# Performance work log

Measured on AMD Instinct MI355X. Metric: run time of the kernel, lower is better.

## Reference

```python
import jax, jax.numpy as jnp
import numpy as np

N_NODES = 100000
N_EDGES = 1600000
D = 128
L = 3


def setup_inputs() -> dict:
    key = jax.random.key(0)
    ks = jax.random.split(key, 5)
    x = jax.random.normal(ks[0], (N_NODES, D), dtype=jnp.float32)
    # Xavier-ish scale for stability through 3 layers
    scale = 1.0 / np.sqrt(D)
    W_self = jax.random.normal(ks[1], (L, D, D), dtype=jnp.float32) * scale
    W_neigh = jax.random.normal(ks[2], (L, D, D), dtype=jnp.float32) * scale
    bias = jnp.zeros((L, D), dtype=jnp.float32)
    src = jax.random.randint(ks[3], (N_EDGES,), 0, N_NODES)
    dst = jax.random.randint(ks[4], (N_EDGES,), 0, N_NODES)
    return {"x": x, "W_self": W_self, "W_neigh": W_neigh, "bias": bias,
            "src": src, "dst": dst}


def reference(x, W_self, W_neigh, bias, src, dst):
    """HomoSAGEEncoder forward (inference mode, dropout = identity).

    Each layer: DGL SAGEConv('mean'):
        h_neigh[v] = mean_{u in in-neighbors(v)} h[u]   (0 if no neighbors)
        h = h @ W_self + h_neigh @ W_neigh + bias
    followed by ReLU.
    """
    N = x.shape[0]
    n_layers = W_self.shape[0]
    # in-degree per destination node (shared across layers)
    deg = jax.ops.segment_sum(jnp.ones_like(dst, dtype=x.dtype), dst,
                              num_segments=N)
    inv_deg = (1.0 / jnp.maximum(deg, 1.0))[:, None]  # [N,1]

    h = x
    for l in range(n_layers):
        msg = h[src]  # [E,D] gather
        h_neigh = jax.ops.segment_sum(msg, dst, num_segments=N) * inv_deg
        h = h @ W_self[l] + h_neigh @ W_neigh[l] + bias[l]
        h = jax.nn.relu(h)
        # dropout is identity at inference; skipped
    return h
```

## Files before the change

### kernel.cpp

```cpp
#include <hip/hip_runtime.h>

typedef __attribute__((ext_vector_type(8))) short short8;
typedef __attribute__((ext_vector_type(4))) float f32x4;

static constexpr int NN = 100000;
static constexpr int NE = 1600000;
static constexpr int DD = 128;
static constexpr int NBUCK = 196;
static constexpr int CAP = 9216;

static constexpr int OFF_GCUR  = 0;
static constexpr int OFF_BBASE = 256;
static constexpr int OFF_OFFS  = 512;
static constexpr int OFF_INV   = 100516;
static constexpr int OFF_WT    = 200520;
static constexpr int OFF_SS    = 249680;
static constexpr int OFF_HB    = 1849680;
static constexpr int OFF_HNB   = 8249680;

__device__ inline ushort f2b(float f) {
  uint u = __builtin_bit_cast(uint, f);
  uint r = (u + 0x7fffu + ((u >> 16) & 1u)) >> 16;
  return (ushort)r;
}
__device__ inline float b2f(ushort b) {
  uint u = ((uint)b) << 16;
  return __builtin_bit_cast(float, u);
}

__global__ void k_zero(int* p) {
  int i = blockIdx.x * blockDim.x + threadIdx.x;
  if (i < 256) p[i] = 0;
}

__global__ void k_x2b(const float* __restrict__ x, ushort* __restrict__ hb) {
  int i = blockIdx.x * blockDim.x + threadIdx.x;
  if (i < NN * (DD / 2)) {
    float2 v = *(const float2*)(x + (size_t)i * 2);
    uint p = (uint)f2b(v.x) | ((uint)f2b(v.y) << 16);
    *(uint*)(hb + (size_t)i * 2) = p;
  }
}

__global__ void k_wt(const float* __restrict__ Ws, const float* __restrict__ Wn,
                     ushort* __restrict__ WtP) {
  int i = blockIdx.x * blockDim.x + threadIdx.x;
  if (i < 3 * 8 * 128 * 32) {
    int j = i & 7;
    int kg = (i >> 3) & 3;
    int col = (i >> 5) & 127;
    int kt = (i >> 12) & 7;
    int l = i >> 15;
    int k = kt * 32 + kg * 8 + j;
    float v = (k < 128) ? Ws[((size_t)l * 128 + k) * 128 + col]
                        : Wn[((size_t)l * 128 + (k - 128)) * 128 + col];
    WtP[i] = f2b(v);
  }
}

__global__ __launch_bounds__(256) void k_bucket(const int* __restrict__ src,
                                                const int* __restrict__ dst,
                                                int* __restrict__ gcur,
                                                int2* __restrict__ ebuf) {
  __shared__ int cnt[NBUCK], base[NBUCK];
  int t = threadIdx.x;
  int b0 = blockIdx.x * 4096;
  if (t < NBUCK) cnt[t] = 0;
  __syncthreads();
  int dv[16], pv[16];
#pragma unroll
  for (int j = 0; j < 16; ++j) {
    int idx = b0 + j * 256 + t;
    if (idx < NE) {
      int d = dst[idx];
      dv[j] = d;
      pv[j] = atomicAdd(&cnt[d >> 9], 1);
    } else dv[j] = -1;
  }
  __syncthreads();
  if (t < NBUCK) base[t] = atomicAdd(&gcur[t], cnt[t]);
  __syncthreads();
#pragma unroll
  for (int j = 0; j < 16; ++j) {
    if (dv[j] >= 0) {
      int idx = b0 + j * 256 + t;
      int b = dv[j] >> 9;
      int2 pr; pr.x = src[idx]; pr.y = dv[j];
      ebuf[(size_t)b * CAP + base[b] + pv[j]] = pr;
    }
  }
}

__global__ void k_bscan(const int* __restrict__ gcur, int* __restrict__ bbase) {
  __shared__ int sc[256];
  int t = threadIdx.x;
  int v = (t < NBUCK) ? gcur[t] : 0;
  sc[t] = v;
  __syncthreads();
  for (int off = 1; off < 256; off <<= 1) {
    int u = (t >= off) ? sc[t - off] : 0;
    __syncthreads();
    sc[t] += u;
    __syncthreads();
  }
  if (t < NBUCK) bbase[t] = sc[t] - v;
  if (t == 255) bbase[NBUCK] = sc[255];
}

__global__ __launch_bounds__(256) void k_sort(const int2* __restrict__ ebuf,
                                              const int* __restrict__ bbase,
                                              int* __restrict__ offs,
                                              float* __restrict__ inv,
                                              int* __restrict__ ss) {
  __shared__ int cnt[512];
  __shared__ int sbase[512];
  __shared__ int scan[256];
  __shared__ int sarr[CAP];
  int b = blockIdx.x, t = threadIdx.x;
  int base0 = bbase[b];
  int n = bbase[b + 1] - base0;
  cnt[t] = 0; cnt[t + 256] = 0;
  __syncthreads();
  const int2* eb = ebuf + (size_t)b * CAP;
  for (int i = t; i < n; i += 256) atomicAdd(&cnt[eb[i].y & 511], 1);
  __syncthreads();
  int c0 = cnt[2 * t], c1 = cnt[2 * t + 1];
  int s = c0 + c1;
  scan[t] = s;
  __syncthreads();
  for (int off = 1; off < 256; off <<= 1) {
    int u = (t >= off) ? scan[t - off] : 0;
    __syncthreads();
    scan[t] += u;
    __syncthreads();
  }
  int eb2 = scan[t] - s;
  sbase[2 * t] = eb2;
  sbase[2 * t + 1] = eb2 + c0;
  int g0 = b * 512 + 2 * t, g1 = g0 + 1;
  if (g0 < NN) {
    offs[g0] = base0 + eb2;
    inv[g0] = 1.0f / (float)(c0 > 1 ? c0 : 1);
  }
  if (g1 < NN) {
    offs[g1] = base0 + eb2 + c0;
    inv[g1] = 1.0f / (float)(c1 > 1 ? c1 : 1);
  }
  if (b == NBUCK - 1 && t == 0) offs[NN] = NE;
  cnt[2 * t] = 0; cnt[2 * t + 1] = 0;
  __syncthreads();
  for (int i = t; i < n; i += 256) {
    int2 e = eb[i];
    int ln = e.y & 511;
    int p = sbase[ln] + atomicAdd(&cnt[ln], 1);
    sarr[p] = e.x;
  }
  __syncthreads();
  for (int i = t; i < n; i += 256) ss[base0 + i] = sarr[i];
}

__global__ __launch_bounds__(256) void k_agg3(const ushort* __restrict__ h,
                                              const int* __restrict__ offs,
                                              const int* __restrict__ ss,
                                              const float* __restrict__ inv_deg,
                                              ushort* __restrict__ hN) {
  int gid = blockIdx.x * blockDim.x + threadIdx.x;
  int wid = gid >> 6;
  int lane = threadIdx.x & 63;
  int q = lane >> 4, l16 = lane & 15;
  int v = wid * 4 + q;
  int beg = offs[v], end = offs[v + 1];
  float a0 = 0, a1 = 0, a2 = 0, a3 = 0, a4 = 0, a5 = 0, a6 = 0, a7 = 0;
  const ushort* hp = h + (size_t)l16 * 8;
#define ACC8(u) { a0 += b2f((ushort)u.x); a1 += b2f((ushort)(u.x >> 16)); \
                  a2 += b2f((ushort)u.y); a3 += b2f((ushort)(u.y >> 16)); \
                  a4 += b2f((ushort)u.z); a5 += b2f((ushort)(u.z >> 16)); \
                  a6 += b2f((ushort)u.w); a7 += b2f((ushort)(u.w >> 16)); }
  int e = beg;
  for (; e + 7 < end; e += 8) {
    uint4 u0 = *(const uint4*)(hp + (size_t)ss[e + 0] * DD);
    uint4 u1 = *(const uint4*)(hp + (size_t)ss[e + 1] * DD);
    uint4 u2 = *(const uint4*)(hp + (size_t)ss[e + 2] * DD);
    uint4 u3 = *(const uint4*)(hp + (size_t)ss[e + 3] * DD);
    uint4 u4 = *(const uint4*)(hp + (size_t)ss[e + 4] * DD);
    uint4 u5 = *(const uint4*)(hp + (size_t)ss[e + 5] * DD);
    uint4 u6 = *(const uint4*)(hp + (size_t)ss[e + 6] * DD);
    uint4 u7 = *(const uint4*)(hp + (size_t)ss[e + 7] * DD);
    ACC8(u0) ACC8(u1) ACC8(u2) ACC8(u3) ACC8(u4) ACC8(u5) ACC8(u6) ACC8(u7)
  }
  for (; e < end; ++e) {
    uint4 u0 = *(const uint4*)(hp + (size_t)ss[e] * DD);
    ACC8(u0)
  }
#undef ACC8
  float w = inv_deg[v];
  a0 *= w; a1 *= w; a2 *= w; a3 *= w; a4 *= w; a5 *= w; a6 *= w; a7 *= w;
  uint4 p;
  p.x = (uint)f2b(a0) | ((uint)f2b(a1) << 16);
  p.y = (uint)f2b(a2) | ((uint)f2b(a3) << 16);
  p.z = (uint)f2b(a4) | ((uint)f2b(a5) << 16);
  p.w = (uint)f2b(a6) | ((uint)f2b(a7) << 16);
  *(uint4*)(hN + (size_t)v * DD + l16 * 8) = p;
}

__global__ __launch_bounds__(256) void k_gemm2(
    const ushort* __restrict__ hA, const ushort* __restrict__ hNb,
    const ushort* __restrict__ WtP, const float* __restrict__ bias,
    ushort* __restrict__ hOutB, float* __restrict__ outF, int writeF) {
  int w = threadIdx.x >> 6;
  int lane = threadIdx.x & 63;
  int r = lane & 15, kg = lane >> 4;
  int colbase = w * 32;

  short8 bfrag[8][2];
#pragma unroll
  for (int kt = 0; kt < 8; ++kt)
#pragma unroll
    for (int nt = 0; nt < 2; ++nt) {
      int col = colbase + nt * 16 + r;
      bfrag[kt][nt] = *(const short8*)(WtP + ((size_t)(kt * 128 + col) * 4 + kg) * 8);
    }

  float bv[2];
  bv[0] = bias[colbase + r];
  bv[1] = bias[colbase + 16 + r];

  int rowblk = blockIdx.x * 128;
#pragma unroll 1
  for (int half = 0; half < 2; ++half) {
    f32x4 acc[2][2][2];
#pragma unroll
    for (int it = 0; it < 2; ++it) {
      int row0 = rowblk + half * 64 + it * 32;
      int ra0 = row0 + r;      if (ra0 > NN - 1) ra0 = NN - 1;
      int ra1 = row0 + 16 + r; if (ra1 > NN - 1) ra1 = NN - 1;
#pragma unroll
      for (int mt = 0; mt < 2; ++mt)
#pragma unroll
        for (int nt = 0; nt < 2; ++nt) acc[it][mt][nt] = (f32x4)0.f;
#pragma unroll
      for (int kt = 0; kt < 8; ++kt) {
        const ushort* hs = (kt < 4) ? hA : hNb;
        int kk = (kt & 3) * 32 + kg * 8;
        short8 a0 = *(const short8*)(hs + (size_t)ra0 * DD + kk);
        short8 a1 = *(const short8*)(hs + (size_t)ra1 * DD + kk);
        acc[it][0][0] = __builtin_amdgcn_mfma_f32_16x16x32_bf16(a0, bfrag[kt][0], acc[it][0][0], 0, 0, 0);
        acc[it][0][1] = __builtin_amdgcn_mfma_f32_16x16x32_bf16(a0, bfrag[kt][1], acc[it][0][1], 0, 0, 0);
        acc[it][1][0] = __builtin_amdgcn_mfma_f32_16x16x32_bf16(a1, bfrag[kt][0], acc[it][1][0], 0, 0, 0);
        acc[it][1][1] = __builtin_amdgcn_mfma_f32_16x16x32_bf16(a1, bfrag[kt][1], acc[it][1][1], 0, 0, 0);
      }
    }
    __syncthreads();
#pragma unroll
    for (int it = 0; it < 2; ++it) {
      int row0 = rowblk + half * 64 + it * 32;
#pragma unroll
      for (int mt = 0; mt < 2; ++mt) {
#pragma unroll
        for (int j = 0; j < 4; ++j) {
          int row = row0 + mt * 16 + kg * 4 + j;
          if (row < NN) {
#pragma unroll
            for (int nt = 0; nt < 2; ++nt) {
              float val = fmaxf(acc[it][mt][nt][j] + bv[nt], 0.f);
              int col = colbase + nt * 16 + r;
              hOutB[(size_t)row * DD + col] = f2b(val);
              if (writeF) outF[(size_t)row * DD + col] = val;
            }
          }
        }
      }
    }
    __syncthreads();
  }
}

extern "C" void kernel_launch(void* const* d_in, const int* in_sizes, int n_in,
                              void* d_out, int out_size, void* d_ws, size_t ws_size,
                              hipStream_t stream) {
  const float* x    = (const float*)d_in[0];
  const float* Ws   = (const float*)d_in[1];
  const float* Wn   = (const float*)d_in[2];
  const float* bias = (const float*)d_in[3];
  const int*   src  = (const int*)d_in[4];
  const int*   dst  = (const int*)d_in[5];
  float* out = (float*)d_out;

  int* ws      = (int*)d_ws;
  int* gcur    = ws + OFF_GCUR;
  int* bbase   = ws + OFF_BBASE;
  int* offs    = ws + OFF_OFFS;
  float* inv   = (float*)(ws + OFF_INV);
  ushort* WtP  = (ushort*)(ws + OFF_WT);
  int* ssorted = ws + OFF_SS;
  ushort* hB   = (ushort*)(ws + OFF_HB);
  ushort* hNb  = (ushort*)(ws + OFF_HNB);
  int2* ebuf   = (int2*)(ws + OFF_HNB);

  k_zero<<<1, 256, 0, stream>>>(gcur);
  k_x2b<<<(NN * (DD / 2) + 255) / 256, 256, 0, stream>>>(x, hB);
  k_wt<<<(3 * 8 * 128 * 32 + 255) / 256, 256, 0, stream>>>(Ws, Wn, WtP);
  k_bucket<<<(NE + 4095) / 4096, 256, 0, stream>>>(src, dst, gcur, ebuf);
  k_bscan<<<1, 256, 0, stream>>>(gcur, bbase);
  k_sort<<<NBUCK, 256, 0, stream>>>(ebuf, bbase, offs, inv, ssorted);

  for (int l = 0; l < 3; ++l) {
    k_agg3<<<NN / 4 / 4, 256, 0, stream>>>(hB, offs, ssorted, inv, hNb);
    k_gemm2<<<(NN + 127) / 128, 256, 0, stream>>>(
        hB, hNb, WtP + (size_t)l * 8 * 128 * 32, bias + l * DD, hB, out, l == 2 ? 1 : 0);
  }
}
```

Before: 531.3 us.

## Fuse neighbor aggregation into GEMM via LDS and merge setup kernels

```diff
diff --git a/kernel.cpp b/kernel.cpp
--- a/kernel.cpp
+++ b/kernel.cpp
@@ -9,14 +9,13 @@
 static constexpr int NBUCK = 196;
 static constexpr int CAP = 9216;
 
-static constexpr int OFF_GCUR  = 0;
-static constexpr int OFF_BBASE = 256;
-static constexpr int OFF_OFFS  = 512;
-static constexpr int OFF_INV   = 100516;
-static constexpr int OFF_WT    = 200520;
-static constexpr int OFF_SS    = 249680;
-static constexpr int OFF_HB    = 1849680;
-static constexpr int OFF_HNB   = 8249680;
+static constexpr int OFF_GCUR = 0;
+static constexpr int OFF_OFFS = 512;
+static constexpr int OFF_INV  = 100516;
+static constexpr int OFF_WT   = 200520;
+static constexpr int OFF_SS   = 249680;
+static constexpr int OFF_HB   = 1849680;
+static constexpr int OFF_HC   = 8249680;
 
 __device__ inline ushort f2b(float f) {
   uint u = __builtin_bit_cast(uint, f);
@@ -28,24 +27,22 @@
   return __builtin_bit_cast(float, u);
 }
 
-__global__ void k_zero(int* p) {
-  int i = blockIdx.x * blockDim.x + threadIdx.x;
-  if (i < 256) p[i] = 0;
-}
-
-__global__ void k_x2b(const float* __restrict__ x, ushort* __restrict__ hb) {
-  int i = blockIdx.x * blockDim.x + threadIdx.x;
-  if (i < NN * (DD / 2)) {
-    float2 v = *(const float2*)(x + (size_t)i * 2);
-    uint p = (uint)f2b(v.x) | ((uint)f2b(v.y) << 16);
-    *(uint*)(hb + (size_t)i * 2) = p;
-  }
-}
-
-__global__ void k_wt(const float* __restrict__ Ws, const float* __restrict__ Wn,
-                     ushort* __restrict__ WtP) {
-  int i = blockIdx.x * blockDim.x + threadIdx.x;
-  if (i < 3 * 8 * 128 * 32) {
+__global__ __launch_bounds__(256) void k_pre(const float* __restrict__ x,
+                                             const float* __restrict__ Ws,
+                                             const float* __restrict__ Wn,
+                                             ushort* __restrict__ hb,
+                                             ushort* __restrict__ WtP,
+                                             int* __restrict__ gcur) {
+  int b = blockIdx.x, t = threadIdx.x;
+  if (b < 12500) {
+    int i = b * 256 + t;
+    float4 v = *(const float4*)(x + (size_t)i * 4);
+    uint2 p;
+    p.x = (uint)f2b(v.x) | ((uint)f2b(v.y) << 16);
+    p.y = (uint)f2b(v.z) | ((uint)f2b(v.w) << 16);
+    *(uint2*)(hb + (size_t)i * 4) = p;
+  } else if (b < 12884) {
+    int i = (b - 12500) * 256 + t;
     int j = i & 7;
     int kg = (i >> 3) & 3;
     int col = (i >> 5) & 127;
@@ -55,6 +52,8 @@
     float v = (k < 128) ? Ws[((size_t)l * 128 + k) * 128 + col]
                         : Wn[((size_t)l * 128 + (k - 128)) * 128 + col];
     WtP[i] = f2b(v);
+  } else {
+    gcur[t] = 0;
   }
 }
 
@@ -91,24 +90,8 @@
   }
 }
 
-__global__ void k_bscan(const int* __restrict__ gcur, int* __restrict__ bbase) {
-  __shared__ int sc[256];
-  int t = threadIdx.x;
-  int v = (t < NBUCK) ? gcur[t] : 0;
-  sc[t] = v;
-  __syncthreads();
-  for (int off = 1; off < 256; off <<= 1) {
-    int u = (t >= off) ? sc[t - off] : 0;
-    __syncthreads();
-    sc[t] += u;
-    __syncthreads();
-  }
-  if (t < NBUCK) bbase[t] = sc[t] - v;
-  if (t == 255) bbase[NBUCK] = sc[255];
-}
-
 __global__ __launch_bounds__(256) void k_sort(const int2* __restrict__ ebuf,
-                                              const int* __restrict__ bbase,
+                                              const int* __restrict__ gcur,
                                               int* __restrict__ offs,
                                               float* __restrict__ inv,
                                               int* __restrict__ ss) {
@@ -117,8 +100,18 @@
   __shared__ int scan[256];
   __shared__ int sarr[CAP];
   int b = blockIdx.x, t = threadIdx.x;
-  int base0 = bbase[b];
-  int n = bbase[b + 1] - base0;
+  int gv = (t < NBUCK) ? gcur[t] : 0;
+  scan[t] = gv;
+  __syncthreads();
+  for (int off = 1; off < 256; off <<= 1) {
+    int u = (t >= off) ? scan[t - off] : 0;
+    __syncthreads();
+    scan[t] += u;
+    __syncthreads();
+  }
+  int nB = gcur[b];
+  int base0 = scan[b] - nB;
+  int n = nB;
   cnt[t] = 0; cnt[t + 256] = 0;
   __syncthreads();
   const int2* eb = ebuf + (size_t)b * CAP;
@@ -159,120 +152,121 @@
   for (int i = t; i < n; i += 256) ss[base0 + i] = sarr[i];
 }
 
-__global__ __launch_bounds__(256) void k_agg3(const ushort* __restrict__ h,
-                                              const int* __restrict__ offs,
-                                              const int* __restrict__ ss,
-                                              const float* __restrict__ inv_deg,
-                                              ushort* __restrict__ hN) {
-  int gid = blockIdx.x * blockDim.x + threadIdx.x;
-  int wid = gid >> 6;
-  int lane = threadIdx.x & 63;
-  int q = lane >> 4, l16 = lane & 15;
-  int v = wid * 4 + q;
-  int beg = offs[v], end = offs[v + 1];
-  float a0 = 0, a1 = 0, a2 = 0, a3 = 0, a4 = 0, a5 = 0, a6 = 0, a7 = 0;
-  const ushort* hp = h + (size_t)l16 * 8;
+__global__ __launch_bounds__(256) void k_fused(
+    const ushort* __restrict__ hIn, const int* __restrict__ offs,
+    const int* __restrict__ ss, const float* __restrict__ inv_deg,
+    const ushort* __restrict__ WtP, const float* __restrict__ bias,
+    ushort* __restrict__ hOut, float* __restrict__ outF, int writeF) {
+  __shared__ ushort hN[128 * 128];
+  int t = threadIdx.x;
+  int w = t >> 6, lane = t & 63;
+  int r = lane & 15, kg = lane >> 4;
+  int row0 = blockIdx.x * 128;
+
+  int colbase = w * 32;
+  short8 bfrag[8][2];
+#pragma unroll
+  for (int kt = 0; kt < 8; ++kt)
+#pragma unroll
+    for (int nt = 0; nt < 2; ++nt) {
+      int col = colbase + nt * 16 + r;
+      bfrag[kt][nt] = *(const short8*)(WtP + ((size_t)(kt * 128 + col) * 4 + kg) * 8);
+    }
+  float bv[2];
+  bv[0] = bias[colbase + r];
+  bv[1] = bias[colbase + 16 + r];
+
+  const ushort* hp = hIn + (size_t)r * 8;
+#pragma unroll 1
+  for (int g = 0; g < 8; ++g) {
+    int lr = w * 32 + g * 4 + kg;
+    int v = row0 + lr;
+    float a0 = 0, a1 = 0, a2 = 0, a3 = 0, a4 = 0, a5 = 0, a6 = 0, a7 = 0;
+    if (v < NN) {
+      int beg = offs[v], end = offs[v + 1];
 #define ACC8(u) { a0 += b2f((ushort)u.x); a1 += b2f((ushort)(u.x >> 16)); \
                   a2 += b2f((ushort)u.y); a3 += b2f((ushort)(u.y >> 16)); \
                   a4 += b2f((ushort)u.z); a5 += b2f((ushort)(u.z >> 16)); \
                   a6 += b2f((ushort)u.w); a7 += b2f((ushort)(u.w >> 16)); }
-  int e = beg;
-  for (; e + 7 < end; e += 8) {
-    uint4 u0 = *(const uint4*)(hp + (size_t)ss[e + 0] * DD);
-    uint4 u1 = *(const uint4*)(hp + (size_t)ss[e + 1] * DD);
-    uint4 u2 = *(const uint4*)(hp + (size_t)ss[e + 2] * DD);
-    uint4 u3 = *(const uint4*)(hp + (size_t)ss[e + 3] * DD);
-    uint4 u4 = *(const uint4*)(hp + (size_t)ss[e + 4] * DD);
-    uint4 u5 = *(const uint4*)(hp + (size_t)ss[e + 5] * DD);
-    uint4 u6 = *(const uint4*)(hp + (size_t)ss[e + 6] * DD);
-    uint4 u7 = *(const uint4*)(hp + (size_t)ss[e + 7] * DD);
-    ACC8(u0) ACC8(u1) ACC8(u2) ACC8(u3) ACC8(u4) ACC8(u5) ACC8(u6) ACC8(u7)
-  }
-  for (; e < end; ++e) {
-    uint4 u0 = *(const uint4*)(hp + (size_t)ss[e] * DD);
-    ACC8(u0)
-  }
+      int e = beg;
+      for (; e + 7 < end; e += 8) {
+        uint4 u0 = *(const uint4*)(hp + (size_t)ss[e + 0] * DD);
+        uint4 u1 = *(const uint4*)(hp + (size_t)ss[e + 1] * DD);
+        uint4 u2 = *(const uint4*)(hp + (size_t)ss[e + 2] * DD);
+        uint4 u3 = *(const uint4*)(hp + (size_t)ss[e + 3] * DD);
+        uint4 u4 = *(const uint4*)(hp + (size_t)ss[e + 4] * DD);
+        uint4 u5 = *(const uint4*)(hp + (size_t)ss[e + 5] * DD);
+        uint4 u6 = *(const uint4*)(hp + (size_t)ss[e + 6] * DD);
+        uint4 u7 = *(const uint4*)(hp + (size_t)ss[e + 7] * DD);
+        ACC8(u0) ACC8(u1) ACC8(u2) ACC8(u3) ACC8(u4) ACC8(u5) ACC8(u6) ACC8(u7)
+      }
+      for (; e < end; ++e) {
+        uint4 u0 = *(const uint4*)(hp + (size_t)ss[e] * DD);
+        ACC8(u0)
+      }
 #undef ACC8
-  float w = inv_deg[v];
-  a0 *= w; a1 *= w; a2 *= w; a3 *= w; a4 *= w; a5 *= w; a6 *= w; a7 *= w;
-  uint4 p;
-  p.x = (uint)f2b(a0) | ((uint)f2b(a1) << 16);
-  p.y = (uint)f2b(a2) | ((uint)f2b(a3) << 16);
-  p.z = (uint)f2b(a4) | ((uint)f2b(a5) << 16);
-  p.w = (uint)f2b(a6) | ((uint)f2b(a7) << 16);
-  *(uint4*)(hN + (size_t)v * DD + l16 * 8) = p;
-}
-
-__global__ __launch_bounds__(256) void k_gemm2(
-    const ushort* __restrict__ hA, const ushort* __restrict__ hNb,
-    const ushort* __restrict__ WtP, const float* __restrict__ bias,
-    ushort* __restrict__ hOutB, float* __restrict__ outF, int writeF) {
-  int w = threadIdx.x >> 6;
-  int lane = threadIdx.x & 63;
-  int r = lane & 15, kg = lane >> 4;
-  int colbase = w * 32;
-
-  short8 bfrag[8][2];
-#pragma unroll
-  for (int kt = 0; kt < 8; ++kt)
-#pragma unroll
-    for (int nt = 0; nt < 2; ++nt) {
-      int col = colbase + nt * 16 + r;
-      bfrag[kt][nt] = *(const short8*)(WtP + ((size_t)(kt * 128 + col) * 4 + kg) * 8);
+      float sc = inv_deg[v];
+      a0 *= sc; a1 *= sc; a2 *= sc; a3 *= sc;
+      a4 *= sc; a5 *= sc; a6 *= sc; a7 *= sc;
     }
-
-  float bv[2];
-  bv[0] = bias[colbase + r];
-  bv[1] = bias[colbase + 16 + r];
-
-  int rowblk = blockIdx.x * 128;
-#pragma unroll 1
-  for (int half = 0; half < 2; ++half) {
-    f32x4 acc[2][2][2];
-#pragma unroll
-    for (int it = 0; it < 2; ++it) {
-      int row0 = rowblk + half * 64 + it * 32;
-      int ra0 = row0 + r;      if (ra0 > NN - 1) ra0 = NN - 1;
-      int ra1 = row0 + 16 + r; if (ra1 > NN - 1) ra1 = NN - 1;
-#pragma unroll
-      for (int mt = 0; mt < 2; ++mt)
-#pragma unroll
-        for (int nt = 0; nt < 2; ++nt) acc[it][mt][nt] = (f32x4)0.f;
-#pragma unroll
-      for (int kt = 0; kt < 8; ++kt) {
-        const ushort* hs = (kt < 4) ? hA : hNb;
-        int kk = (kt & 3) * 32 + kg * 8;
-        short8 a0 = *(const short8*)(hs + (size_t)ra0 * DD + kk);
-        short8 a1 = *(const short8*)(hs + (size_t)ra1 * DD + kk);
-        acc[it][0][0] = __builtin_amdgcn_mfma_f32_16x16x32_bf16(a0, bfrag[kt][0], acc[it][0][0], 0, 0, 0);
-        acc[it][0][1] = __builtin_amdgcn_mfma_f32_16x16x32_bf16(a0, bfrag[kt][1], acc[it][0][1], 0, 0, 0);
-        acc[it][1][0] = __builtin_amdgcn_mfma_f32_16x16x32_bf16(a1, bfrag[kt][0], acc[it][1][0], 0, 0, 0);
-        acc[it][1][1] = __builtin_amdgcn_mfma_f32_16x16x32_bf16(a1, bfrag[kt][1], acc[it][1][1], 0, 0, 0);
+    uint4 p;
+    p.x = (uint)f2b(a0) | ((uint)f2b(a1) << 16);
+    p.y = (uint)f2b(a2) | ((uint)f2b(a3) << 16);
+    p.z = (uint)f2b(a4) | ((uint)f2b(a5) << 16);
+    p.w = (uint)f2b(a6) | ((uint)f2b(a7) << 16);
+    *(uint4*)((char*)hN + lr * 256 + ((r * 16) ^ ((lr & 7) << 4))) = p;
+  }
+  __syncthreads();
+
+  f32x4 acc[4][2][2];
+#pragma unroll
+  for (int it = 0; it < 4; ++it)
+#pragma unroll
+    for (int mt = 0; mt < 2; ++mt)
+#pragma unroll
+      for (int nt = 0; nt < 2; ++nt) acc[it][mt][nt] = (f32x4)0.f;
+
+#pragma unroll
+  for (int it = 0; it < 4; ++it) {
+    int lr0 = it * 32 + r, lr1 = lr0 + 16;
+    int ra0 = row0 + lr0; if (ra0 > NN - 1) ra0 = NN - 1;
+    int ra1 = row0 + lr1; if (ra1 > NN - 1) ra1 = NN - 1;
+#pragma unroll
+    for (int kt = 0; kt < 8; ++kt) {
+      short8 a0, a1;
+      if (kt < 4) {
+        int kk = kt * 32 + kg * 8;
+        a0 = *(const short8*)(hIn + (size_t)ra0 * DD + kk);
+        a1 = *(const short8*)(hIn + (size_t)ra1 * DD + kk);
+      } else {
+        int bo = (kt & 3) * 64 + kg * 16;
+        a0 = *(const short8*)((char*)hN + lr0 * 256 + (bo ^ ((lr0 & 7) << 4)));
+        a1 = *(const short8*)((char*)hN + lr1 * 256 + (bo ^ ((lr1 & 7) << 4)));
       }
+      acc[it][0][0] = __builtin_amdgcn_mfma_f32_16x16x32_bf16(a0, bfrag[kt][0], acc[it][0][0], 0, 0, 0);
+      acc[it][0][1] = __builtin_amdgcn_mfma_f32_16x16x32_bf16(a0, bfrag[kt][1], acc[it][0][1], 0, 0, 0);
+      acc[it][1][0] = __builtin_amdgcn_mfma_f32_16x16x32_bf16(a1, bfrag[kt][0], acc[it][1][0], 0, 0, 0);
+      acc[it][1][1] = __builtin_amdgcn_mfma_f32_16x16x32_bf16(a1, bfrag[kt][1], acc[it][1][1], 0, 0, 0);
     }
-    __syncthreads();
-#pragma unroll
-    for (int it = 0; it < 2; ++it) {
-      int row0 = rowblk + half * 64 + it * 32;
-#pragma unroll
-      for (int mt = 0; mt < 2; ++mt) {
-#pragma unroll
-        for (int j = 0; j < 4; ++j) {
-          int row = row0 + mt * 16 + kg * 4 + j;
-          if (row < NN) {
-#pragma unroll
-            for (int nt = 0; nt < 2; ++nt) {
-              float val = fmaxf(acc[it][mt][nt][j] + bv[nt], 0.f);
-              int col = colbase + nt * 16 + r;
-              hOutB[(size_t)row * DD + col] = f2b(val);
-              if (writeF) outF[(size_t)row * DD + col] = val;
-            }
+  }
+
+#pragma unroll
+  for (int it = 0; it < 4; ++it)
+#pragma unroll
+    for (int mt = 0; mt < 2; ++mt)
+#pragma unroll
+      for (int j = 0; j < 4; ++j) {
+        int row = row0 + it * 32 + mt * 16 + kg * 4 + j;
+        if (row < NN) {
+#pragma unroll
+          for (int nt = 0; nt < 2; ++nt) {
+            float val = fmaxf(acc[it][mt][nt][j] + bv[nt], 0.f);
+            int col = colbase + nt * 16 + r;
+            if (writeF) outF[(size_t)row * DD + col] = val;
+            else        hOut[(size_t)row * DD + col] = f2b(val);
           }
         }
       }
-    }
-    __syncthreads();
-  }
 }
 
 extern "C" void kernel_launch(void* const* d_in, const int* in_sizes, int n_in,
@@ -288,25 +282,26 @@
 
   int* ws      = (int*)d_ws;
   int* gcur    = ws + OFF_GCUR;
-  int* bbase   = ws + OFF_BBASE;
   int* offs    = ws + OFF_OFFS;
   float* inv   = (float*)(ws + OFF_INV);
   ushort* WtP  = (ushort*)(ws + OFF_WT);
   int* ssorted = ws + OFF_SS;
   ushort* hB   = (ushort*)(ws + OFF_HB);
-  ushort* hNb  = (ushort*)(ws + OFF_HNB);
-  int2* ebuf   = (int2*)(ws + OFF_HNB);
-
-  k_zero<<<1, 256, 0, stream>>>(gcur);
-  k_x2b<<<(NN * (DD / 2) + 255) / 256, 256, 0, stream>>>(x, hB);
-  k_wt<<<(3 * 8 * 128 * 32 + 255) / 256, 256, 0, stream>>>(Ws, Wn, WtP);
+  ushort* hC   = (ushort*)(ws + OFF_HC);
+  int2* ebuf   = (int2*)(ws + OFF_HC);
+
+  k_pre<<<12885, 256, 0, stream>>>(x, Ws, Wn, hB, WtP, gcur);
   k_bucket<<<(NE + 4095) / 4096, 256, 0, stream>>>(src, dst, gcur, ebuf);
-  k_bscan<<<1, 256, 0, stream>>>(gcur, bbase);
-  k_sort<<<NBUCK, 256, 0, stream>>>(ebuf, bbase, offs, inv, ssorted);
-
+  k_sort<<<NBUCK, 256, 0, stream>>>(ebuf, gcur, offs, inv, ssorted);
+
+  const ushort* hcur = hB;
+  ushort* hnext = hC;
   for (int l = 0; l < 3; ++l) {
-    k_agg3<<<NN / 4 / 4, 256, 0, stream>>>(hB, offs, ssorted, inv, hNb);
-    k_gemm2<<<(NN + 127) / 128, 256, 0, stream>>>(
-        hB, hNb, WtP + (size_t)l * 8 * 128 * 32, bias + l * DD, hB, out, l == 2 ? 1 : 0);
-  }
-}
+    k_fused<<<(NN + 127) / 128, 256, 0, stream>>>(
+        hcur, offs, ssorted, inv, WtP + (size_t)l * 8 * 128 * 32,
+        bias + l * DD, hnext, out, l == 2 ? 1 : 0);
+    const ushort* tmp = hnext;
+    hnext = (ushort*)hcur;
+    hcur = tmp;
+  }
+}
```

New measurement: 569.8 us. +7.2%, slower.
